# Kernel optimization log

Measured on AMD Instinct MI355X. Metric: run time of the kernel, lower is better.

Reference implementation:

```python
import jax, jax.numpy as jnp
import numpy as np

N = 50000
E = 600000
D = 128
HEADS = 4
G = 64  # num graphs
EPS = 1e-5


def setup_inputs() -> dict:
    key = jax.random.key(0)
    ks = jax.random.split(key, 16)
    s = 0.05
    inp = {
        'x': jax.random.normal(ks[0], (N, D), jnp.float32),
        'edge_index': jax.random.randint(ks[1], (2, E), 0, N, jnp.int64),
        'batch': jnp.sort(jax.random.randint(ks[2], (N,), 0, G, jnp.int64)),
        # GCN layer 1
        'W1': jax.random.normal(ks[3], (D, D), jnp.float32) * s,
        'b1': jnp.zeros((D,), jnp.float32),
        'g1': jnp.ones((D,), jnp.float32),
        'beta1': jnp.zeros((D,), jnp.float32),
        # GCN layer 2
        'W2': jax.random.normal(ks[4], (D, D), jnp.float32) * s,
        'b2': jnp.zeros((D,), jnp.float32),
        'g2': jnp.ones((D,), jnp.float32),
        'beta2': jnp.zeros((D,), jnp.float32),
        # GAT (heads=4, concat=False -> mean over heads)
        'gat_W': jax.random.normal(ks[5], (D, HEADS * D), jnp.float32) * s,
        'att_src': jax.random.normal(ks[6], (HEADS, D), jnp.float32) * s,
        'att_dst': jax.random.normal(ks[7], (HEADS, D), jnp.float32) * s,
        'gat_b': jnp.zeros((D,), jnp.float32),
    }
    return inp


def _layer_norm(x, g, b):
    mu = jnp.mean(x, axis=-1, keepdims=True)
    var = jnp.mean((x - mu) ** 2, axis=-1, keepdims=True)
    return (x - mu) * jax.lax.rsqrt(var + EPS) * g + b


def _gcn(x, W, b, src, dst, deg_inv_sqrt):
    h = x @ W                                    # [N, D]
    norm = deg_inv_sqrt[src] * deg_inv_sqrt[dst]  # [E']
    msg = norm[:, None] * h[src]                 # [E', D] gather
    return jax.ops.segment_sum(msg, dst, num_segments=N) + b


def _gat(x, W, b, att_src, att_dst, src, dst):
    h = (x @ W).reshape(N, HEADS, D)             # [N, H, D]
    a_s = jnp.einsum('nhd,hd->nh', h, att_src)   # [N, H]
    a_d = jnp.einsum('nhd,hd->nh', h, att_dst)
    e = jax.nn.leaky_relu(a_s[src] + a_d[dst], 0.2)          # [E', H]
    m = jax.ops.segment_max(e, dst, num_segments=N)          # segment softmax
    ex = jnp.exp(e - m[dst])
    den = jax.ops.segment_sum(ex, dst, num_segments=N)
    alpha = ex / den[dst]                                     # [E', H]
    out = jax.ops.segment_sum(alpha[:, :, None] * h[src], dst, num_segments=N)
    return jnp.mean(out, axis=1) + b             # concat=False -> head mean


def reference(x, edge_index, batch, W1, b1, g1, beta1, W2, b2, g2, beta2,
              gat_W, gat_b, att_src, att_dst):
    # add self loops (PyG default for GCNConv and GATConv)
    loops = jnp.arange(N, dtype=edge_index.dtype)
    src = jnp.concatenate([edge_index[0], loops])
    dst = jnp.concatenate([edge_index[1], loops])
    deg = jax.ops.segment_sum(jnp.ones_like(dst, jnp.float32), dst, num_segments=N)
    deg_inv_sqrt = jnp.where(deg > 0, jax.lax.rsqrt(jnp.maximum(deg, 1.0)), 0.0)

    # GCN stack: conv -> LayerNorm -> relu -> dropout(eval=identity)
    h = jax.nn.relu(_layer_norm(_gcn(x, W1, b1, src, dst, deg_inv_sqrt), g1, beta1))
    h = jax.nn.relu(_layer_norm(_gcn(h, W2, b2, src, dst, deg_inv_sqrt), g2, beta2))

    h = jax.nn.relu(_gat(h, gat_W, gat_b, att_src, att_dst, src, dst))
    node_embeddings = h

    cnt = jax.ops.segment_sum(jnp.ones((N,), jnp.float32), batch, num_segments=G)
    mean_pool = jax.ops.segment_sum(h, batch, num_segments=G) / jnp.maximum(cnt, 1.0)[:, None]
    max_pool = jax.ops.segment_max(h, batch, num_segments=G)
    graph_embedding = jnp.concatenate([mean_pool, max_pool], axis=1)  # [G, 2D]
    return graph_embedding, node_embeddings
```

## Files before the change

### kernel.cpp

```cpp
#include <hip/hip_runtime.h>
#include <math.h>


#define TPB 256

typedef __attribute__((ext_vector_type(8))) short short8;
typedef __attribute__((ext_vector_type(4))) float f32x4;
union U4S8 { uint4 u; short8 s; };

__device__ __forceinline__ float lrelu(float x) { return x > 0.f ? x : 0.2f * x; }

__device__ __forceinline__ unsigned short f2bf(float f) {
    unsigned int u = __float_as_uint(f);
    u += 0x7fffu + ((u >> 16) & 1u);
    return (unsigned short)(u >> 16);
}
__device__ __forceinline__ float2 bf2x(unsigned int u) {
    return make_float2(__uint_as_float(u << 16), __uint_as_float(u & 0xffff0000u));
}
__device__ __forceinline__ float sel4(float4 v, int h) {
    float r = v.x;
    r = (h == 1) ? v.y : r;
    r = (h == 2) ? v.z : r;
    r = (h == 3) ? v.w : r;
    return r;
}

__global__ __launch_bounds__(TPB) void k_hist(const int* __restrict__ dst,
                                              int* __restrict__ deg, int e) {
    int i = blockIdx.x * TPB + threadIdx.x;
    if (i < e) atomicAdd(&deg[dst[i]], 1);
}

__global__ __launch_bounds__(TPB) void k_scan_part(const int* __restrict__ deg,
                                                   int* __restrict__ part, int n) {
    int i = blockIdx.x * TPB + threadIdx.x;
    int v = (i < n) ? deg[i] : 0;
#pragma unroll
    for (int o = 32; o > 0; o >>= 1) v += __shfl_xor(v, o);
    __shared__ int sw[4];
    if ((threadIdx.x & 63) == 0) sw[threadIdx.x >> 6] = v;
    __syncthreads();
    if (threadIdx.x == 0) part[blockIdx.x] = sw[0] + sw[1] + sw[2] + sw[3];
}

__global__ __launch_bounds__(TPB) void k_scan_top(int* __restrict__ part, int nb) {
    __shared__ int sm[TPB];
    int t = threadIdx.x;
    int v = (t < nb) ? part[t] : 0;
    sm[t] = v;
    __syncthreads();
    for (int off = 1; off < TPB; off <<= 1) {
        int u = (t >= off) ? sm[t - off] : 0;
        __syncthreads();
        sm[t] += u;
        __syncthreads();
    }
    if (t < nb) part[t] = sm[t] - v;
}

__global__ __launch_bounds__(TPB) void k_scan_apply(const int* __restrict__ deg,
                                                    const int* __restrict__ part,
                                                    int* __restrict__ row_start,
                                                    int* __restrict__ cursor,
                                                    float* __restrict__ dis,
                                                    int n, int e_total) {
    __shared__ int sm[TPB];
    int i = blockIdx.x * TPB + threadIdx.x;
    int t = threadIdx.x;
    int d = (i < n) ? deg[i] : 0;
    sm[t] = d;
    __syncthreads();
    for (int off = 1; off < TPB; off <<= 1) {
        int u = (t >= off) ? sm[t - off] : 0;
        __syncthreads();
        sm[t] += u;
        __syncthreads();
    }
    if (i < n) {
        int rs = part[blockIdx.x] + sm[t] - d;
        row_start[i] = rs;
        cursor[i] = rs;
        dis[i] = rsqrtf((float)(d + 1));
    }
    if (blockIdx.x == 0 && t == 0) row_start[n] = e_total;
}

__global__ __launch_bounds__(TPB) void k_scatter(const int* __restrict__ src,
                                                 const int* __restrict__ dst,
                                                 int* __restrict__ cursor,
                                                 int* __restrict__ csr_src, int e) {
    int i = blockIdx.x * TPB + threadIdx.x;
    if (i < e) {
        int p = atomicAdd(&cursor[dst[i]], 1);
        csr_src[p] = src[i];
    }
}

__global__ __launch_bounds__(TPB) void k_f2bf(const float* __restrict__ in,
                                              unsigned short* __restrict__ out, int n4) {
    int i = blockIdx.x * TPB + threadIdx.x;
    if (i >= n4) return;
    float4 v = ((const float4*)in)[i];
    unsigned int p0 = (unsigned int)f2bf(v.x) | ((unsigned int)f2bf(v.y) << 16);
    unsigned int p1 = (unsigned int)f2bf(v.z) | ((unsigned int)f2bf(v.w) << 16);
    ((uint2*)out)[i] = make_uint2(p0, p1);
}

__global__ __launch_bounds__(TPB) void k_wt(const float* __restrict__ W,
                                            unsigned short* __restrict__ Wt, int ocols) {
    int i = blockIdx.x * TPB + threadIdx.x;
    if (i >= 128 * ocols) return;
    int k = i / ocols, n = i - k * ocols;
    Wt[n * 128 + k] = f2bf(W[i]);
}

__global__ __launch_bounds__(TPB, 2) void k_gemm_mfma(const unsigned short* __restrict__ feat,
                                                      const unsigned short* __restrict__ Wt,
                                                      unsigned short* __restrict__ C,
                                                      int nrows, int ocols) {
    __shared__ uint4 wl[2048];
    int t = threadIdx.x;
    int cb = blockIdx.y << 7;
#pragma unroll
    for (int i = 0; i < 8; ++i) {
        int fi = i * 256 + t;
        int l = fi & 63, ct = (fi >> 6) & 7, ks = fi >> 9;
        int chan = cb + ct * 16 + (l & 15);
        wl[fi] = ((const uint4*)(Wt + (size_t)chan * 128))[ks * 4 + (l >> 4)];
    }
    __syncthreads();

    int wave = t >> 6, lane = t & 63;
    int wr = wave >> 1, wc = wave & 1;
    int nbase = (blockIdx.x << 7) + (wc << 6);
    const uint4* brow[4];
#pragma unroll
    for (int nt = 0; nt < 4; ++nt) {
        int node = nbase + nt * 16 + (lane & 15);
        node = node < nrows ? node : (nrows - 1);
        brow[nt] = (const uint4*)(feat + (size_t)node * 128);
    }
    f32x4 acc[4][4];
#pragma unroll
    for (int mt = 0; mt < 4; ++mt)
#pragma unroll
        for (int nt = 0; nt < 4; ++nt) acc[mt][nt] = (f32x4)0.f;

    int kq = lane >> 4;
#pragma unroll
    for (int ks = 0; ks < 4; ++ks) {
        U4S8 a[4], b[4];
#pragma unroll
        for (int mt = 0; mt < 4; ++mt)
            a[mt].u = wl[(ks * 8 + wr * 4 + mt) * 64 + lane];
#pragma unroll
        for (int nt = 0; nt < 4; ++nt)
            b[nt].u = brow[nt][ks * 4 + kq];
#pragma unroll
        for (int mt = 0; mt < 4; ++mt)
#pragma unroll
            for (int nt = 0; nt < 4; ++nt)
                acc[mt][nt] = __builtin_amdgcn_mfma_f32_16x16x32_bf16(
                    a[mt].s, b[nt].s, acc[mt][nt], 0, 0, 0);
    }
#pragma unroll
    for (int nt = 0; nt < 4; ++nt) {
        int node = nbase + nt * 16 + (lane & 15);
        if (node >= nrows) continue;
#pragma unroll
        for (int mt = 0; mt < 4; ++mt) {
            int chan = cb + (wr << 6) + mt * 16 + (lane >> 4) * 4;
            f32x4 v = acc[mt][nt];
            unsigned int p0 = (unsigned int)f2bf(v.x) | ((unsigned int)f2bf(v.y) << 16);
            unsigned int p1 = (unsigned int)f2bf(v.z) | ((unsigned int)f2bf(v.w) << 16);
            *(uint2*)(C + (size_t)node * ocols + chan) = make_uint2(p0, p1);
        }
    }
}

__global__ __launch_bounds__(TPB) void k_gcn_fused(const unsigned short* __restrict__ hb,
                                                   const int* __restrict__ csr_src,
                                                   const int* __restrict__ row_start,
                                                   const float* __restrict__ dis,
                                                   const float* __restrict__ b,
                                                   const float* __restrict__ g,
                                                   const float* __restrict__ beta,
                                                   unsigned short* __restrict__ out, int n) {
    __shared__ int   ssrc[4][64];
    __shared__ float swt[4][64];
    int node = (blockIdx.x * TPB + threadIdx.x) >> 6;
    int lane = threadIdx.x & 63;
    int wid = threadIdx.x >> 6;
    if (node >= n) return;
    int s0 = row_start[node], s1 = row_start[node + 1];
    float dn = dis[node];
    const unsigned int* hu = (const unsigned int*)hb;
    float2 acc = make_float2(0.f, 0.f);
    for (int base = s0; base < s1; base += 64) {
        int cnt = min(64, s1 - base);
        int sidx = 0; float w = 0.f;
        if (lane < cnt) { sidx = csr_src[base + lane]; w = dis[sidx]; }
        ssrc[wid][lane] = sidx;
        swt[wid][lane] = w;
        for (int j = 0; j < cnt; ++j) {
            int s = ssrc[wid][j];
            float wj = swt[wid][j];
            float2 v = bf2x(hu[(size_t)s * 64 + lane]);
            acc.x += wj * v.x;
            acc.y += wj * v.y;
        }
    }
    float sl = dn * dn;
    float2 hv = bf2x(hu[(size_t)node * 64 + lane]);
    float2 bv = ((const float2*)b)[lane];
    float vx = dn * acc.x + sl * hv.x + bv.x;
    float vy = dn * acc.y + sl * hv.y + bv.y;
    float s = vx + vy, sq = vx * vx + vy * vy;
#pragma unroll
    for (int o = 32; o > 0; o >>= 1) {
        s  += __shfl_xor(s, o);
        sq += __shfl_xor(sq, o);
    }
    float mu = s * (1.f / 128.f);
    float var = sq * (1.f / 128.f) - mu * mu;
    float rstd = rsqrtf(var + 1e-5f);
    float2 gv  = ((const float2*)g)[lane];
    float2 btv = ((const float2*)beta)[lane];
    float ox = fmaxf((vx - mu) * rstd * gv.x + btv.x, 0.f);
    float oy = fmaxf((vy - mu) * rstd * gv.y + btv.y, 0.f);
    ((unsigned int*)out)[(size_t)node * 64 + lane] =
        (unsigned int)f2bf(ox) | ((unsigned int)f2bf(oy) << 16);
}

__global__ __launch_bounds__(TPB) void k_att_dots(const unsigned short* __restrict__ hgb,
                                                  const float* __restrict__ att_s,
                                                  const float* __restrict__ att_d,
                                                  float* __restrict__ a_s,
                                                  float* __restrict__ a_d, int n) {
    int wave = (blockIdx.x * TPB + threadIdx.x) >> 6;
    int lane = threadIdx.x & 63;
    if (wave >= n) return;
    int h = lane >> 4, j = lane & 15;
    const uint4* hq = (const uint4*)hgb;
    uint4 u = hq[(size_t)wave * 64 + lane];
    float2 p0 = bf2x(u.x), p1 = bf2x(u.y), p2 = bf2x(u.z), p3 = bf2x(u.w);
    const float4* s4 = (const float4*)(att_s + h * 128 + j * 8);
    const float4* d4 = (const float4*)(att_d + h * 128 + j * 8);
    float4 s0 = s4[0], s1 = s4[1];
    float4 d0 = d4[0], d1 = d4[1];
    float ps = p0.x * s0.x + p0.y * s0.y + p1.x * s0.z + p1.y * s0.w
             + p2.x * s1.x + p2.y * s1.y + p3.x * s1.z + p3.y * s1.w;
    float pd = p0.x * d0.x + p0.y * d0.y + p1.x * d0.z + p1.y * d0.w
             + p2.x * d1.x + p2.y * d1.y + p3.x * d1.z + p3.y * d1.w;
#pragma unroll
    for (int o = 8; o > 0; o >>= 1) {
        ps += __shfl_xor(ps, o);
        pd += __shfl_xor(pd, o);
    }
    if (j == 0) {
        a_s[wave * 4 + h] = ps;
        a_d[wave * 4 + h] = pd;
    }
}

__global__ __launch_bounds__(TPB) void k_gat_fused(const unsigned short* __restrict__ hgb,
                                                   const float* __restrict__ a_s,
                                                   const float* __restrict__ a_d,
                                                   const int* __restrict__ csr_src,
                                                   const int* __restrict__ row_start,
                                                   float* __restrict__ out, int n) {
    __shared__ int   ssrc[4][64];
    __shared__ float swt[4][4][65];
    int node = (blockIdx.x * TPB + threadIdx.x) >> 6;
    int lane = threadIdx.x & 63;
    int wid = threadIdx.x >> 6;
    if (node >= n) return;
    int s0 = row_start[node], s1 = row_start[node + 1];
    int h = lane >> 4;
    const float4* as4 = (const float4*)a_s;
    float4 ad = ((const float4*)a_d)[node];
    float4 asn = as4[node];
    float4 wself;
    wself.x = __expf(lrelu(asn.x + ad.x));
    wself.y = __expf(lrelu(asn.y + ad.y));
    wself.z = __expf(lrelu(asn.z + ad.z));
    wself.w = __expf(lrelu(asn.w + ad.w));
    const uint4* hq = (const uint4*)hgb;
    float acc[8];
    {
        float wsh = sel4(wself, h);
        uint4 u = hq[(size_t)node * 64 + lane];
        float2 p0 = bf2x(u.x), p1 = bf2x(u.y), p2 = bf2x(u.z), p3 = bf2x(u.w);
        acc[0] = wsh * p0.x; acc[1] = wsh * p0.y;
        acc[2] = wsh * p1.x; acc[3] = wsh * p1.y;
        acc[4] = wsh * p2.x; acc[5] = wsh * p2.y;
        acc[6] = wsh * p3.x; acc[7] = wsh * p3.y;
    }
    float4 den = make_float4(0.f, 0.f, 0.f, 0.f);
    for (int base = s0; base < s1; base += 64) {
        int cnt = min(64, s1 - base);
        int sidx = 0;
        float4 w4 = make_float4(0.f, 0.f, 0.f, 0.f);
        if (lane < cnt) {
            sidx = csr_src[base + lane];
            float4 a = as4[sidx];
            w4.x = __expf(lrelu(a.x + ad.x));
            w4.y = __expf(lrelu(a.y + ad.y));
            w4.z = __expf(lrelu(a.z + ad.z));
            w4.w = __expf(lrelu(a.w + ad.w));
            den.x += w4.x; den.y += w4.y; den.z += w4.z; den.w += w4.w;
        }
        ssrc[wid][lane] = sidx;
        swt[wid][0][lane] = w4.x;
        swt[wid][1][lane] = w4.y;
        swt[wid][2][lane] = w4.z;
        swt[wid][3][lane] = w4.w;
        for (int j = 0; j < cnt; ++j) {
            int s = ssrc[wid][j];
            float wj = swt[wid][h][j];
            uint4 u = hq[(size_t)s * 64 + lane];
            float2 p0 = bf2x(u.x), p1 = bf2x(u.y), p2 = bf2x(u.z), p3 = bf2x(u.w);
            acc[0] += wj * p0.x; acc[1] += wj * p0.y;
            acc[2] += wj * p1.x; acc[3] += wj * p1.y;
            acc[4] += wj * p2.x; acc[5] += wj * p2.y;
            acc[6] += wj * p3.x; acc[7] += wj * p3.y;
        }
    }
#pragma unroll
    for (int o = 32; o > 0; o >>= 1) {
        den.x += __shfl_xor(den.x, o);
        den.y += __shfl_xor(den.y, o);
        den.z += __shfl_xor(den.z, o);
        den.w += __shfl_xor(den.w, o);
    }
    den.x += wself.x; den.y += wself.y; den.z += wself.z; den.w += wself.w;
    float winv = 0.25f / sel4(den, h);
#pragma unroll
    for (int j = 0; j < 8; ++j) acc[j] *= winv;
#pragma unroll
    for (int j = 0; j < 8; ++j) acc[j] += __shfl_xor(acc[j], 16);
#pragma unroll
    for (int j = 0; j < 8; ++j) acc[j] += __shfl_xor(acc[j], 32);
    if (lane < 16) {
        float4* o4 = (float4*)(out + (size_t)node * 128 + lane * 8);
        o4[0] = make_float4(acc[0], acc[1], acc[2], acc[3]);
        o4[1] = make_float4(acc[4], acc[5], acc[6], acc[7]);
    }
}

__global__ __launch_bounds__(TPB) void k_final_pool(const float* __restrict__ acc,
                                                    const float* __restrict__ gat_b,
                                                    const int* __restrict__ batch,
                                                    float* __restrict__ node_out,
                                                    float* __restrict__ mean_acc,
                                                    float* __restrict__ max_acc,
                                                    float* __restrict__ cnt, int n) {
    int wave = (blockIdx.x * TPB + threadIdx.x) >> 6;
    int lane = threadIdx.x & 63;
    int n0 = wave * 16;
    if (n0 >= n) return;
    int n1 = min(n0 + 16, n);
    float2 bv = ((const float2*)gat_b)[lane];
    float2 bsum = make_float2(0.f, 0.f), bmax = make_float2(0.f, 0.f);
    int cur_g = batch[n0];
    int cntloc = 0;
    for (int nn = n0; nn < n1; ++nn) {
        int g = batch[nn];
        if (g != cur_g) {
            float* ma = mean_acc + cur_g * 128 + lane * 2;
            atomicAdd(ma + 0, bsum.x);
            atomicAdd(ma + 1, bsum.y);
            int* mxp = (int*)(max_acc + cur_g * 128 + lane * 2);
            atomicMax(mxp + 0, __float_as_int(bmax.x));
            atomicMax(mxp + 1, __float_as_int(bmax.y));
            if (lane == 0) atomicAdd(&cnt[cur_g], (float)cntloc);
            bsum = make_float2(0.f, 0.f);
            bmax = make_float2(0.f, 0.f);
            cntloc = 0;
            cur_g = g;
        }
        float2 a = ((const float2*)acc)[nn * 64 + lane];
        float2 o = make_float2(fmaxf(a.x + bv.x, 0.f), fmaxf(a.y + bv.y, 0.f));
        ((float2*)node_out)[nn * 64 + lane] = o;
        bsum.x += o.x; bsum.y += o.y;
        bmax.x = fmaxf(bmax.x, o.x); bmax.y = fmaxf(bmax.y, o.y);
        ++cntloc;
    }
    float* ma = mean_acc + cur_g * 128 + lane * 2;
    atomicAdd(ma + 0, bsum.x);
    atomicAdd(ma + 1, bsum.y);
    int* mxp = (int*)(max_acc + cur_g * 128 + lane * 2);
    atomicMax(mxp + 0, __float_as_int(bmax.x));
    atomicMax(mxp + 1, __float_as_int(bmax.y));
    if (lane == 0) atomicAdd(&cnt[cur_g], (float)cntloc);
}

__global__ __launch_bounds__(TPB) void k_pool_final(const float* __restrict__ mean_acc,
                                                    const float* __restrict__ max_acc,
                                                    const float* __restrict__ cnt,
                                                    float* __restrict__ gout, int g128) {
    int i = blockIdx.x * TPB + threadIdx.x;
    if (i >= g128) return;
    int g = i >> 7, d = i & 127;
    float c = fmaxf(cnt[g], 1.f);
    gout[g * 256 + d] = mean_acc[i] / c;
    gout[g * 256 + 128 + d] = max_acc[i];
}

extern "C" void kernel_launch(void* const* d_in, const int* in_sizes, int n_in,
                              void* d_out, int out_size, void* d_ws, size_t ws_size,
                              hipStream_t stream) {
    const float* x       = (const float*)d_in[0];
    const int*   ei      = (const int*)d_in[1];
    const int*   batch   = (const int*)d_in[2];
    const float* W1      = (const float*)d_in[3];
    const float* b1      = (const float*)d_in[4];
    const float* g1      = (const float*)d_in[5];
    const float* beta1   = (const float*)d_in[6];
    const float* W2      = (const float*)d_in[7];
    const float* b2      = (const float*)d_in[8];
    const float* g2      = (const float*)d_in[9];
    const float* beta2   = (const float*)d_in[10];
    const float* gat_W   = (const float*)d_in[11];
    const float* att_src = (const float*)d_in[12];
    const float* att_dst = (const float*)d_in[13];
    const float* gat_b   = (const float*)d_in[14];

    const int N = in_sizes[0] / 128;
    const int E = in_sizes[1] / 2;
    const int G = (out_size - N * 128) / 256;
    const int* src = ei;
    const int* dst = ei + E;

    float* ws = (float*)d_ws;
    float* dis      = ws; ws += N;
    float* Bf       = ws; ws += (size_t)N * 128;
    float* a_s      = ws; ws += N * 4;
    float* a_d      = ws; ws += N * 4;
    float* mean_acc = ws; ws += G * 128;
    float* max_acc  = ws; ws += G * 128;
    float* cnt      = ws; ws += G;
    unsigned short* xb  = (unsigned short*)ws; ws += (size_t)N * 64;
    unsigned short* Hbf = (unsigned short*)ws; ws += (size_t)N * 64;
    unsigned short* Bbf = (unsigned short*)ws; ws += (size_t)N * 64;
    unsigned short* Cbf = (unsigned short*)ws; ws += (size_t)N * 64;
    unsigned short* hgb = (unsigned short*)ws; ws += (size_t)N * 256;
    unsigned short* Wt1 = (unsigned short*)ws; ws += 128 * 64;
    unsigned short* Wt2 = (unsigned short*)ws; ws += 128 * 64;
    unsigned short* Wtg = (unsigned short*)ws; ws += 512 * 64;
    int* deg       = (int*)ws; ws += N;
    int* part      = (int*)ws; ws += 256;
    int* row_start = (int*)ws; ws += N + 1;
    int* cursor    = (int*)ws; ws += N + 1;
    int* csr_src   = (int*)ws; ws += E;

    float* gout = (float*)d_out;
    float* node_out = gout + G * 256;

    auto cdiv = [](long a, long b) { return (int)((a + b - 1) / b); };
    const int nb = cdiv(N, TPB);

    hipMemsetAsync(deg, 0, (size_t)N * 4, stream);
    k_hist<<<cdiv(E, TPB), TPB, 0, stream>>>(dst, deg, E);
    k_scan_part<<<nb, TPB, 0, stream>>>(deg, part, N);
    k_scan_top<<<1, TPB, 0, stream>>>(part, nb);
    k_scan_apply<<<nb, TPB, 0, stream>>>(deg, part, row_start, cursor, dis, N, E);
    k_scatter<<<cdiv(E, TPB), TPB, 0, stream>>>(src, dst, cursor, csr_src, E);

    k_f2bf<<<cdiv((long)N * 32, TPB), TPB, 0, stream>>>(x, xb, N * 32);
    k_wt<<<cdiv(128 * 128, TPB), TPB, 0, stream>>>(W1, Wt1, 128);
    k_wt<<<cdiv(128 * 128, TPB), TPB, 0, stream>>>(W2, Wt2, 128);
    k_wt<<<cdiv(128 * 512, TPB), TPB, 0, stream>>>(gat_W, Wtg, 512);

    k_gemm_mfma<<<dim3(cdiv(N, 128), 1), TPB, 0, stream>>>(xb, Wt1, Hbf, N, 128);
    k_gcn_fused<<<cdiv((long)N * 64, TPB), TPB, 0, stream>>>(Hbf, csr_src, row_start, dis,
                                                             b1, g1, beta1, Bbf, N);
    k_gemm_mfma<<<dim3(cdiv(N, 128), 1), TPB, 0, stream>>>(Bbf, Wt2, Hbf, N, 128);
    k_gcn_fused<<<cdiv((long)N * 64, TPB), TPB, 0, stream>>>(Hbf, csr_src, row_start, dis,
                                                             b2, g2, beta2, Cbf, N);
    k_gemm_mfma<<<dim3(cdiv(N, 128), 4), TPB, 0, stream>>>(Cbf, Wtg, hgb, N, 512);
    k_att_dots<<<cdiv((long)N * 64, TPB), TPB, 0, stream>>>(hgb, att_src, att_dst, a_s, a_d, N);
    k_gat_fused<<<cdiv((long)N * 64, TPB), TPB, 0, stream>>>(hgb, a_s, a_d, csr_src, row_start, Bf, N);

    hipMemsetAsync(mean_acc, 0, (size_t)(G * 256 + G) * 4, stream);
    k_final_pool<<<cdiv((long)cdiv(N, 16) * 64, TPB), TPB, 0, stream>>>(Bf, gat_b, batch, node_out,
                                                                        mean_acc, max_acc, cnt, N);
    k_pool_final<<<cdiv((long)G * 128, TPB), TPB, 0, stream>>>(mean_acc, max_acc, cnt, gout, G * 128);
}
```

Measured before the change: 454.7 us.

## Widen GCN gathers to 16-byte loads, unroll GAT gather, fuse bias+relu into GAT

The GCN aggregation kernel now has each quarter-wave gather a different neighbor row with uint4 loads, processing four edges per iteration. Partial sums are reduced across quarters with shuffles before LayerNorm. The GAT gather loop is unrolled by four so several independent row loads are in flight at once. Bias add and ReLU move into the GAT kernel, which writes node_out directly, so the pooling kernel only reads it and the fp32 intermediate buffer goes away. The cost is more registers and shuffle work, plus masked lanes when a node's degree is not a multiple of four.

Result: no change. 455.3 us (+0.1%).

```diff
diff --git a/kernel.cpp b/kernel.cpp
--- a/kernel.cpp
+++ b/kernel.cpp
@@ -195,42 +195,77 @@
     if (node >= n) return;
     int s0 = row_start[node], s1 = row_start[node + 1];
     float dn = dis[node];
-    const unsigned int* hu = (const unsigned int*)hb;
-    float2 acc = make_float2(0.f, 0.f);
+    const uint4* hq = (const uint4*)hb;
+    int q = lane >> 4, fl = lane & 15;
+    float acc[8];
+#pragma unroll
+    for (int i = 0; i < 8; ++i) acc[i] = 0.f;
     for (int base = s0; base < s1; base += 64) {
         int cnt = min(64, s1 - base);
         int sidx = 0; float w = 0.f;
         if (lane < cnt) { sidx = csr_src[base + lane]; w = dis[sidx]; }
         ssrc[wid][lane] = sidx;
         swt[wid][lane] = w;
-        for (int j = 0; j < cnt; ++j) {
-            int s = ssrc[wid][j];
-            float wj = swt[wid][j];
-            float2 v = bf2x(hu[(size_t)s * 64 + lane]);
-            acc.x += wj * v.x;
-            acc.y += wj * v.y;
+        for (int j = 0; j < cnt; j += 4) {
+            int jj = j + q;
+            int ok = jj < cnt;
+            int s = ssrc[wid][ok ? jj : 0];
+            float wj = ok ? swt[wid][jj] : 0.f;
+            uint4 u = hq[(size_t)s * 16 + fl];
+            float2 p0 = bf2x(u.x), p1 = bf2x(u.y), p2 = bf2x(u.z), p3 = bf2x(u.w);
+            acc[0] += wj * p0.x; acc[1] += wj * p0.y;
+            acc[2] += wj * p1.x; acc[3] += wj * p1.y;
+            acc[4] += wj * p2.x; acc[5] += wj * p2.y;
+            acc[6] += wj * p3.x; acc[7] += wj * p3.y;
         }
     }
+#pragma unroll
+    for (int i = 0; i < 8; ++i) {
+        acc[i] += __shfl_xor(acc[i], 16);
+        acc[i] += __shfl_xor(acc[i], 32);
+    }
     float sl = dn * dn;
-    float2 hv = bf2x(hu[(size_t)node * 64 + lane]);
-    float2 bv = ((const float2*)b)[lane];
-    float vx = dn * acc.x + sl * hv.x + bv.x;
-    float vy = dn * acc.y + sl * hv.y + bv.y;
-    float s = vx + vy, sq = vx * vx + vy * vy;
-#pragma unroll
-    for (int o = 32; o > 0; o >>= 1) {
+    uint4 us = hq[(size_t)node * 16 + fl];
+    float2 h0 = bf2x(us.x), h1 = bf2x(us.y), h2 = bf2x(us.z), h3 = bf2x(us.w);
+    float4 b0 = ((const float4*)b)[fl * 2], b1 = ((const float4*)b)[fl * 2 + 1];
+    float v[8];
+    v[0] = dn * acc[0] + sl * h0.x + b0.x;
+    v[1] = dn * acc[1] + sl * h0.y + b0.y;
+    v[2] = dn * acc[2] + sl * h1.x + b0.z;
+    v[3] = dn * acc[3] + sl * h1.y + b0.w;
+    v[4] = dn * acc[4] + sl * h2.x + b1.x;
+    v[5] = dn * acc[5] + sl * h2.y + b1.y;
+    v[6] = dn * acc[6] + sl * h3.x + b1.z;
+    v[7] = dn * acc[7] + sl * h3.y + b1.w;
+    float s = 0.f, sq = 0.f;
+#pragma unroll
+    for (int i = 0; i < 8; ++i) { s += v[i]; sq += v[i] * v[i]; }
+#pragma unroll
+    for (int o = 8; o > 0; o >>= 1) {
         s  += __shfl_xor(s, o);
         sq += __shfl_xor(sq, o);
     }
     float mu = s * (1.f / 128.f);
     float var = sq * (1.f / 128.f) - mu * mu;
     float rstd = rsqrtf(var + 1e-5f);
-    float2 gv  = ((const float2*)g)[lane];
-    float2 btv = ((const float2*)beta)[lane];
-    float ox = fmaxf((vx - mu) * rstd * gv.x + btv.x, 0.f);
-    float oy = fmaxf((vy - mu) * rstd * gv.y + btv.y, 0.f);
-    ((unsigned int*)out)[(size_t)node * 64 + lane] =
-        (unsigned int)f2bf(ox) | ((unsigned int)f2bf(oy) << 16);
+    float4 g0  = ((const float4*)g)[fl * 2],    g1v = ((const float4*)g)[fl * 2 + 1];
+    float4 bt0 = ((const float4*)beta)[fl * 2], bt1 = ((const float4*)beta)[fl * 2 + 1];
+    float o0 = fmaxf((v[0] - mu) * rstd * g0.x + bt0.x, 0.f);
+    float o1 = fmaxf((v[1] - mu) * rstd * g0.y + bt0.y, 0.f);
+    float o2 = fmaxf((v[2] - mu) * rstd * g0.z + bt0.z, 0.f);
+    float o3 = fmaxf((v[3] - mu) * rstd * g0.w + bt0.w, 0.f);
+    float o4 = fmaxf((v[4] - mu) * rstd * g1v.x + bt1.x, 0.f);
+    float o5 = fmaxf((v[5] - mu) * rstd * g1v.y + bt1.y, 0.f);
+    float o6 = fmaxf((v[6] - mu) * rstd * g1v.z + bt1.z, 0.f);
+    float o7 = fmaxf((v[7] - mu) * rstd * g1v.w + bt1.w, 0.f);
+    if (q == 0) {
+        uint4 pk;
+        pk.x = (unsigned int)f2bf(o0) | ((unsigned int)f2bf(o1) << 16);
+        pk.y = (unsigned int)f2bf(o2) | ((unsigned int)f2bf(o3) << 16);
+        pk.z = (unsigned int)f2bf(o4) | ((unsigned int)f2bf(o5) << 16);
+        pk.w = (unsigned int)f2bf(o6) | ((unsigned int)f2bf(o7) << 16);
+        ((uint4*)out)[(size_t)node * 16 + fl] = pk;
+    }
 }
 
 __global__ __launch_bounds__(TPB) void k_att_dots(const unsigned short* __restrict__ hgb,
@@ -269,7 +304,8 @@
                                                    const float* __restrict__ a_d,
                                                    const int* __restrict__ csr_src,
                                                    const int* __restrict__ row_start,
-                                                   float* __restrict__ out, int n) {
+                                                   const float* __restrict__ gat_b,
+                                                   float* __restrict__ node_out, int n) {
     __shared__ int   ssrc[4][64];
     __shared__ float swt[4][4][65];
     int node = (blockIdx.x * TPB + threadIdx.x) >> 6;
@@ -316,7 +352,31 @@
         swt[wid][1][lane] = w4.y;
         swt[wid][2][lane] = w4.z;
         swt[wid][3][lane] = w4.w;
-        for (int j = 0; j < cnt; ++j) {
+        int j = 0;
+        for (; j + 4 <= cnt; j += 4) {
+            int sa = ssrc[wid][j + 0], sb = ssrc[wid][j + 1];
+            int sc = ssrc[wid][j + 2], sd = ssrc[wid][j + 3];
+            float wa = swt[wid][h][j + 0], wb = swt[wid][h][j + 1];
+            float wc = swt[wid][h][j + 2], wd = swt[wid][h][j + 3];
+            uint4 ua = hq[(size_t)sa * 64 + lane];
+            uint4 ub = hq[(size_t)sb * 64 + lane];
+            uint4 uc = hq[(size_t)sc * 64 + lane];
+            uint4 ud = hq[(size_t)sd * 64 + lane];
+            float2 p0, p1, p2, p3;
+            p0 = bf2x(ua.x); p1 = bf2x(ua.y); p2 = bf2x(ua.z); p3 = bf2x(ua.w);
+            acc[0] += wa * p0.x; acc[1] += wa * p0.y; acc[2] += wa * p1.x; acc[3] += wa * p1.y;
+            acc[4] += wa * p2.x; acc[5] += wa * p2.y; acc[6] += wa * p3.x; acc[7] += wa * p3.y;
+            p0 = bf2x(ub.x); p1 = bf2x(ub.y); p2 = bf2x(ub.z); p3 = bf2x(ub.w);
+            acc[0] += wb * p0.x; acc[1] += wb * p0.y; acc[2] += wb * p1.x; acc[3] += wb * p1.y;
+            acc[4] += wb * p2.x; acc[5] += wb * p2.y; acc[6] += wb * p3.x; acc[7] += wb * p3.y;
+            p0 = bf2x(uc.x); p1 = bf2x(uc.y); p2 = bf2x(uc.z); p3 = bf2x(uc.w);
+            acc[0] += wc * p0.x; acc[1] += wc * p0.y; acc[2] += wc * p1.x; acc[3] += wc * p1.y;
+            acc[4] += wc * p2.x; acc[5] += wc * p2.y; acc[6] += wc * p3.x; acc[7] += wc * p3.y;
+            p0 = bf2x(ud.x); p1 = bf2x(ud.y); p2 = bf2x(ud.z); p3 = bf2x(ud.w);
+            acc[0] += wd * p0.x; acc[1] += wd * p0.y; acc[2] += wd * p1.x; acc[3] += wd * p1.y;
+            acc[4] += wd * p2.x; acc[5] += wd * p2.y; acc[6] += wd * p3.x; acc[7] += wd * p3.y;
+        }
+        for (; j < cnt; ++j) {
             int s = ssrc[wid][j];
             float wj = swt[wid][h][j];
             uint4 u = hq[(size_t)s * 64 + lane];
@@ -342,26 +402,27 @@
     for (int j = 0; j < 8; ++j) acc[j] += __shfl_xor(acc[j], 16);
 #pragma unroll
     for (int j = 0; j < 8; ++j) acc[j] += __shfl_xor(acc[j], 32);
+    int fl = lane & 15;
+    float4 gb0 = ((const float4*)gat_b)[fl * 2], gb1 = ((const float4*)gat_b)[fl * 2 + 1];
     if (lane < 16) {
-        float4* o4 = (float4*)(out + (size_t)node * 128 + lane * 8);
-        o4[0] = make_float4(acc[0], acc[1], acc[2], acc[3]);
-        o4[1] = make_float4(acc[4], acc[5], acc[6], acc[7]);
-    }
-}
-
-__global__ __launch_bounds__(TPB) void k_final_pool(const float* __restrict__ acc,
-                                                    const float* __restrict__ gat_b,
-                                                    const int* __restrict__ batch,
-                                                    float* __restrict__ node_out,
-                                                    float* __restrict__ mean_acc,
-                                                    float* __restrict__ max_acc,
-                                                    float* __restrict__ cnt, int n) {
+        float4* o4 = (float4*)(node_out + (size_t)node * 128 + fl * 8);
+        o4[0] = make_float4(fmaxf(acc[0] + gb0.x, 0.f), fmaxf(acc[1] + gb0.y, 0.f),
+                            fmaxf(acc[2] + gb0.z, 0.f), fmaxf(acc[3] + gb0.w, 0.f));
+        o4[1] = make_float4(fmaxf(acc[4] + gb1.x, 0.f), fmaxf(acc[5] + gb1.y, 0.f),
+                            fmaxf(acc[6] + gb1.z, 0.f), fmaxf(acc[7] + gb1.w, 0.f));
+    }
+}
+
+__global__ __launch_bounds__(TPB) void k_pool(const float* __restrict__ node_out,
+                                              const int* __restrict__ batch,
+                                              float* __restrict__ mean_acc,
+                                              float* __restrict__ max_acc,
+                                              float* __restrict__ cnt, int n) {
     int wave = (blockIdx.x * TPB + threadIdx.x) >> 6;
     int lane = threadIdx.x & 63;
     int n0 = wave * 16;
     if (n0 >= n) return;
     int n1 = min(n0 + 16, n);
-    float2 bv = ((const float2*)gat_b)[lane];
     float2 bsum = make_float2(0.f, 0.f), bmax = make_float2(0.f, 0.f);
     int cur_g = batch[n0];
     int cntloc = 0;
@@ -380,9 +441,7 @@
             cntloc = 0;
             cur_g = g;
         }
-        float2 a = ((const float2*)acc)[nn * 64 + lane];
-        float2 o = make_float2(fmaxf(a.x + bv.x, 0.f), fmaxf(a.y + bv.y, 0.f));
-        ((float2*)node_out)[nn * 64 + lane] = o;
+        float2 o = ((const float2*)node_out)[(size_t)nn * 64 + lane];
         bsum.x += o.x; bsum.y += o.y;
         bmax.x = fmaxf(bmax.x, o.x); bmax.y = fmaxf(bmax.y, o.y);
         ++cntloc;
@@ -435,7 +494,6 @@
 
     float* ws = (float*)d_ws;
     float* dis      = ws; ws += N;
-    float* Bf       = ws; ws += (size_t)N * 128;
     float* a_s      = ws; ws += N * 4;
     float* a_d      = ws; ws += N * 4;
     float* mean_acc = ws; ws += G * 128;
@@ -481,10 +539,11 @@
                                                              b2, g2, beta2, Cbf, N);
     k_gemm_mfma<<<dim3(cdiv(N, 128), 4), TPB, 0, stream>>>(Cbf, Wtg, hgb, N, 512);
     k_att_dots<<<cdiv((long)N * 64, TPB), TPB, 0, stream>>>(hgb, att_src, att_dst, a_s, a_d, N);
-    k_gat_fused<<<cdiv((long)N * 64, TPB), TPB, 0, stream>>>(hgb, a_s, a_d, csr_src, row_start, Bf, N);
+    k_gat_fused<<<cdiv((long)N * 64, TPB), TPB, 0, stream>>>(hgb, a_s, a_d, csr_src, row_start,
+                                                             gat_b, node_out, N);
 
     hipMemsetAsync(mean_acc, 0, (size_t)(G * 256 + G) * 4, stream);
-    k_final_pool<<<cdiv((long)cdiv(N, 16) * 64, TPB), TPB, 0, stream>>>(Bf, gat_b, batch, node_out,
-                                                                        mean_acc, max_acc, cnt, N);
+    k_pool<<<cdiv((long)cdiv(N, 16) * 64, TPB), TPB, 0, stream>>>(node_out, batch,
+                                                                  mean_acc, max_acc, cnt, N);
     k_pool_final<<<cdiv((long)G * 128, TPB), TPB, 0, stream>>>(mean_acc, max_acc, cnt, gout, G * 128);
 }
```
